# Performance work log

Hardware: AMD Instinct MI355X
Metric: run time of the kernel (lower is better)

The kernel has to match this reference:

```python
import jax, jax.numpy as jnp
import numpy as np

N_NODES = 100000


def gcn_layer(x, W, b, src, dst, n):
    # PyG GCNConv: add self-loops, symmetric degree normalization,
    # message = norm * (x @ W)[src], aggregated (sum) at dst, plus bias.
    loops = jnp.arange(n, dtype=src.dtype)
    s = jnp.concatenate([src, loops])  # [E+N]
    d = jnp.concatenate([dst, loops])  # [E+N]
    deg = jnp.zeros((n,), x.dtype).at[d].add(jnp.ones((s.shape[0],), x.dtype))
    dinv = jnp.where(deg > 0, jax.lax.rsqrt(deg), 0.0)
    norm = dinv[s] * dinv[d]  # [E+N]
    h = x @ W  # [N, out]
    msg = h[s] * norm[:, None]  # [E+N, out]
    out = jax.ops.segment_sum(msg, d, num_segments=n)
    return out + b


def setup_inputs() -> dict:
    key = jax.random.key(0)
    k1, k2, k3, k4 = jax.random.split(key, 4)
    in_dim, hid_dim, out_dim = 128, 128, 64
    x = jax.random.normal(k1, (N_NODES, in_dim), dtype=jnp.float32)
    edge_index = jax.random.randint(k2, (2, 1600000), 0, N_NODES, dtype=jnp.int64)
    W1 = jax.random.normal(k3, (in_dim, hid_dim), dtype=jnp.float32) / np.sqrt(in_dim)
    b1 = jnp.zeros((hid_dim,), jnp.float32)
    W2 = jax.random.normal(k4, (hid_dim, out_dim), dtype=jnp.float32) / np.sqrt(hid_dim)
    b2 = jnp.zeros((out_dim,), jnp.float32)
    return {"x": x, "edge_index": edge_index, "W1": W1, "b1": b1, "W2": W2, "b2": b2}


def reference(x, edge_index, W1, b1, W2, b2):
    src, dst = edge_index[0], edge_index[1]
    h = gcn_layer(x, W1, b1, src, dst, N_NODES)
    h = jax.nn.relu(h)
    # F.dropout(training=False) -> identity (eval mode reference)
    out = gcn_layer(h, W2, b2, src, dst, N_NODES)
    return out
```

## Files before the change

kernel.cpp:

```cpp
#include <hip/hip_runtime.h>
#include <hip/hip_fp16.h>

#define NN 100000
#define NSB 256
#define WPS2 391
#define CAP2 8192
#define EPB 16

typedef _Float16 f16;
typedef _Float16 f16x8 __attribute__((ext_vector_type(8)));
typedef float f32x4 __attribute__((ext_vector_type(4)));

__device__ __forceinline__ int eload(const void* e, long i, int is64) {
  if (is64) return (int)((const long long*)e)[i];
  return ((const int*)e)[i];
}

__global__ __launch_bounds__(1024) void k_detect(const unsigned* __restrict__ e,
                                                 int* __restrict__ flag,
                                                 int* __restrict__ bcur2) {
  __shared__ unsigned red[1024];
  int t = threadIdx.x;
  if (t < NSB) bcur2[t] = t * CAP2;
  unsigned acc = e[1 + 2 * t] | e[1 + 2 * t + 2048];
  red[t] = acc;
  __syncthreads();
  for (int off = 512; off > 0; off >>= 1) {
    if (t < off) red[t] |= red[t + off];
    __syncthreads();
  }
  if (t == 0) *flag = (red[0] == 0) ? 1 : 0;
}

__global__ void k_wprep(const float* __restrict__ W1, const float* __restrict__ W2,
                        f16* __restrict__ Wt1, f16* __restrict__ Wt2) {
  int idx = blockIdx.x * 256 + threadIdx.x;
  if (idx < 128 * 128) {
    int k = idx / 128, n = idx % 128;
    Wt1[n * 128 + k] = (f16)W1[idx];
  } else {
    int i2 = idx - 128 * 128;
    if (i2 < 128 * 64) {
      int k = i2 / 64, n = i2 % 64;
      Wt2[n * 128 + k] = (f16)W2[i2];
    }
  }
}

__global__ __launch_bounds__(256) void k_split(const void* __restrict__ e,
                                               const int* __restrict__ flag,
                                               int E, int* __restrict__ bcur2,
                                               int* __restrict__ srcb,
                                               int* __restrict__ dstb) {
  __shared__ int hist[NSB];
  const int tid = threadIdx.x;
  const long b0 = (long)blockIdx.x * (256 * EPB);
  const int is64 = *flag;
  hist[tid] = 0;
  __syncthreads();

  int sv[EPB], dv[EPB];
#pragma unroll
  for (int j = 0; j < EPB; ++j) {
    long idx = b0 + j * 256 + tid;
    int s = 0, d = -1;
    if (idx < E) {
      s = eload(e, idx, is64);
      d = eload(e, (long)E + idx, is64);
    }
    sv[j] = s; dv[j] = d;
    if (d >= 0) atomicAdd(&hist[(unsigned)d / WPS2], 1);
  }
  __syncthreads();
  {
    int c = hist[tid];
    int base = (c > 0) ? atomicAdd(&bcur2[tid], c) : 0;
    __syncthreads();
    hist[tid] = base;
  }
  __syncthreads();
#pragma unroll
  for (int j = 0; j < EPB; ++j) {
    int d = dv[j];
    if (d < 0) continue;
    int pos = atomicAdd(&hist[(unsigned)d / WPS2], 1);
    srcb[pos] = sv[j];
    dstb[pos] = d;
  }
}

__global__ __launch_bounds__(256) void k_wscan(const int* __restrict__ bcur2,
                                               int* __restrict__ wbase,
                                               int* __restrict__ rowptr, int E) {
  __shared__ int sm[NSB];
  int t = threadIdx.x;
  int c = bcur2[t] - t * CAP2;
  sm[t] = c;
  __syncthreads();
  for (int off = 1; off < NSB; off <<= 1) {
    int a = (t >= off) ? sm[t - off] : 0;
    __syncthreads();
    sm[t] += a;
    __syncthreads();
  }
  wbase[t] = sm[t] - c;
  if (t == 0) rowptr[NN] = E;
}

__global__ __launch_bounds__(256) void k_build(const int* __restrict__ dstb,
                                               const int* __restrict__ srcb,
                                               const int* __restrict__ bcur2,
                                               const int* __restrict__ wbase,
                                               int* __restrict__ rowptr,
                                               float* __restrict__ dinv,
                                               int* __restrict__ csr) {
  __shared__ int lc[512];
  __shared__ int cur[512];
  const int tid = threadIdx.x;
  const int b = blockIdx.x;
  const int nlo = b * WPS2;
  const int nhi = (nlo + WPS2 < NN) ? nlo + WPS2 : NN;
  const int nw = nhi - nlo;
  lc[tid] = 0; lc[tid + 256] = 0;
  __syncthreads();
  const int cnt = bcur2[b] - b * CAP2;
  const long s0 = (long)b * CAP2;
  for (int i = tid; i < cnt; i += 256)
    atomicAdd(&lc[dstb[s0 + i] - nlo], 1);
  __syncthreads();
  for (int off = 1; off < 512; off <<= 1) {
    int a0 = (tid >= off) ? lc[tid - off] : 0;
    int a1 = (tid + 256 >= off) ? lc[tid + 256 - off] : 0;
    __syncthreads();
    lc[tid] += a0; lc[tid + 256] += a1;
    __syncthreads();
  }
  const int wb = wbase[b];
#pragma unroll
  for (int h = 0; h < 2; ++h) {
    int j = tid + h * 256;
    if (j < nw) {
      int inc = lc[j];
      int c = inc - (j > 0 ? lc[j - 1] : 0);
      int ex = wb + inc - c;
      rowptr[nlo + j] = ex;
      dinv[nlo + j] = rsqrtf((float)c + 1.0f);
      cur[j] = ex;
    }
  }
  __syncthreads();
  for (int i = tid; i < cnt; i += 256) {
    int d = dstb[s0 + i];
    int pos = atomicAdd(&cur[d - nlo], 1);
    csr[pos] = srcb[s0 + i];
  }
}

template <int COUT, bool RELU, typename TIN>
__global__ __launch_bounds__(256) void gemm_mfma(const TIN* __restrict__ X,
                                                 const f16* __restrict__ Wt,
                                                 const float* __restrict__ dinv,
                                                 f16* __restrict__ Y) {
  constexpr int NF = COUT / 16;
  __shared__ f16 Al[128 * 128];
  __shared__ f16 Bl[COUT * 128];
  const int tid = threadIdx.x;
  const long row0 = (long)blockIdx.x * 128;

  for (int c = tid; c < COUT * 16; c += 256) {
    int n = c >> 4, g = c & 15;
    f16x8 v = *(const f16x8*)&Wt[n * 128 + g * 8];
    *(f16x8*)((char*)Bl + n * 256 + ((g * 16) ^ ((n & 7) << 4))) = v;
  }
  for (int c = tid; c < 2048; c += 256) {
    int r = c >> 4, g = c & 15;
    long grow = row0 + r;
    f16x8 v;
    if (grow < NN) {
      if constexpr (sizeof(TIN) == 4) {
        const float4* p = (const float4*)&X[grow * 128 + g * 8];
        float4 p0 = p[0], p1 = p[1];
        float f[8] = {p0.x, p0.y, p0.z, p0.w, p1.x, p1.y, p1.z, p1.w};
#pragma unroll
        for (int j = 0; j < 8; ++j) {
          float t = RELU ? fmaxf(f[j], 0.f) : f[j];
          v[j] = (f16)t;
        }
      } else {
        v = *(const f16x8*)&X[grow * 128 + g * 8];
        if (RELU) {
#pragma unroll
          for (int j = 0; j < 8; ++j) v[j] = v[j] > (f16)0 ? v[j] : (f16)0;
        }
      }
    } else {
#pragma unroll
      for (int j = 0; j < 8; ++j) v[j] = (f16)0;
    }
    *(f16x8*)((char*)Al + r * 256 + ((g * 16) ^ ((r & 7) << 4))) = v;
  }
  __syncthreads();

  const int l = tid & 63, w = tid >> 6;
  const int lm = l & 15, lg = l >> 4;
  const int r0 = w * 32 + lm, r1 = r0 + 16;

  f32x4 acc0[NF], acc1[NF];
#pragma unroll
  for (int nf = 0; nf < NF; ++nf) { acc0[nf] = (f32x4)(0.f); acc1[nf] = (f32x4)(0.f); }

#pragma unroll
  for (int kk = 0; kk < 4; ++kk) {
    const int kb = kk * 64 + lg * 16;
    f16x8 a0 = *(const f16x8*)((const char*)Al + r0 * 256 + (kb ^ ((r0 & 7) << 4)));
    f16x8 a1 = *(const f16x8*)((const char*)Al + r1 * 256 + (kb ^ ((r1 & 7) << 4)));
#pragma unroll
    for (int nf = 0; nf < NF; ++nf) {
      int n = nf * 16 + lm;
      f16x8 b = *(const f16x8*)((const char*)Bl + n * 256 + (kb ^ ((n & 7) << 4)));
      acc0[nf] = __builtin_amdgcn_mfma_f32_16x16x32_f16(a0, b, acc0[nf], 0, 0, 0);
      acc1[nf] = __builtin_amdgcn_mfma_f32_16x16x32_f16(a1, b, acc1[nf], 0, 0, 0);
    }
  }

#pragma unroll
  for (int reg = 0; reg < 4; ++reg) {
    long gr0 = row0 + w * 32 + lg * 4 + reg;
    long gr1 = gr0 + 16;
    float d0 = (gr0 < NN) ? dinv[gr0] : 0.f;
    float d1 = (gr1 < NN) ? dinv[gr1] : 0.f;
#pragma unroll
    for (int nf = 0; nf < NF; ++nf) {
      if (gr0 < NN) Y[gr0 * COUT + nf * 16 + lm] = (f16)(acc0[nf][reg] * d0);
      if (gr1 < NN) Y[gr1 * COUT + nf * 16 + lm] = (f16)(acc1[nf][reg] * d1);
    }
  }
}

__device__ __forceinline__ void acc8f(float* acc, const __half* p) {
  float4 raw = *(const float4*)p;
  const __half2* h = (const __half2*)&raw;
#pragma unroll
  for (int q = 0; q < 4; ++q) {
    float2 f = __half22float2(h[q]);
    acc[2 * q] += f.x; acc[2 * q + 1] += f.y;
  }
}

template <int C, typename TOUT>
__global__ __launch_bounds__(256) void k_agg8(const __half* __restrict__ hn,
                                              const int* __restrict__ rowptr,
                                              const int* __restrict__ csr,
                                              const float* __restrict__ dinv,
                                              const float* __restrict__ bias,
                                              TOUT* __restrict__ out) {
  constexpr int TP = C / 8;
  long t = (long)blockIdx.x * 256 + threadIdx.x;
  int d = (int)(t / TP);
  if (d >= NN) return;
  int c8 = (int)(t % TP) * 8;

  float acc[8] = {0, 0, 0, 0, 0, 0, 0, 0};
  acc8f(acc, &hn[(long)d * C + c8]);
  int e = rowptr[d];
  const int end = rowptr[d + 1];

  for (; e + 8 <= end; e += 8) {
    int s[8];
#pragma unroll
    for (int u = 0; u < 8; ++u) s[u] = csr[e + u];
    float4 r[8];
#pragma unroll
    for (int u = 0; u < 8; ++u) r[u] = *(const float4*)&hn[(long)s[u] * C + c8];
#pragma unroll
    for (int u = 0; u < 8; ++u) {
      const __half2* h = (const __half2*)&r[u];
#pragma unroll
      for (int q = 0; q < 4; ++q) {
        float2 f = __half22float2(h[q]);
        acc[2 * q] += f.x; acc[2 * q + 1] += f.y;
      }
    }
  }
  if (e + 4 <= end) {
    int s[4];
#pragma unroll
    for (int u = 0; u < 4; ++u) s[u] = csr[e + u];
    float4 r[4];
#pragma unroll
    for (int u = 0; u < 4; ++u) r[u] = *(const float4*)&hn[(long)s[u] * C + c8];
#pragma unroll
    for (int u = 0; u < 4; ++u) {
      const __half2* h = (const __half2*)&r[u];
#pragma unroll
      for (int q = 0; q < 4; ++q) {
        float2 f = __half22float2(h[q]);
        acc[2 * q] += f.x; acc[2 * q + 1] += f.y;
      }
    }
    e += 4;
  }
  for (; e < end; ++e) acc8f(acc, &hn[(long)csr[e] * C + c8]);

  float dd = dinv[d];
  float4 bv0 = *(const float4*)&bias[c8];
  float4 bv1 = *(const float4*)&bias[c8 + 4];
  float o[8];
  o[0] = acc[0] * dd + bv0.x; o[1] = acc[1] * dd + bv0.y;
  o[2] = acc[2] * dd + bv0.z; o[3] = acc[3] * dd + bv0.w;
  o[4] = acc[4] * dd + bv1.x; o[5] = acc[5] * dd + bv1.y;
  o[6] = acc[6] * dd + bv1.z; o[7] = acc[7] * dd + bv1.w;

  if constexpr (sizeof(TOUT) == 2) {
    __half2 hp[4];
    hp[0] = __floats2half2_rn(o[0], o[1]);
    hp[1] = __floats2half2_rn(o[2], o[3]);
    hp[2] = __floats2half2_rn(o[4], o[5]);
    hp[3] = __floats2half2_rn(o[6], o[7]);
    *(float4*)&out[(long)d * C + c8] = *(float4*)hp;
  } else {
    *(float4*)&out[(long)d * C + c8]     = make_float4(o[0], o[1], o[2], o[3]);
    *(float4*)&out[(long)d * C + c8 + 4] = make_float4(o[4], o[5], o[6], o[7]);
  }
}

extern "C" void kernel_launch(void* const* d_in, const int* in_sizes, int n_in,
                              void* d_out, int out_size, void* d_ws, size_t ws_size,
                              hipStream_t stream) {
  const float* x  = (const float*)d_in[0];
  const void*  ep = d_in[1];
  const float* W1 = (const float*)d_in[2];
  const float* b1 = (const float*)d_in[3];
  const float* W2 = (const float*)d_in[4];
  const float* b2 = (const float*)d_in[5];
  float* out = (float*)d_out;
  const int E = in_sizes[1] / 2;

  float*  wsf    = (float*)d_ws;
  int*    wsi    = (int*)d_ws;
  int*    flag   = wsi;
  int*    bcur2  = wsi + 64;
  int*    wbase  = wsi + 320;
  float*  dinv   = wsf + 576;
  int*    rowptr = wsi + 100576;
  f16*    Wt1    = (f16*)(wsi + 200640);
  f16*    Wt2    = (f16*)(wsi + 208832);
  int*    csr    = wsi + 212992;
  int*    srcb   = wsi + 1812992;
  int*    dstb   = wsi + 3910144;
  f16*    hn1    = (f16*)(wsi + 6007296);
  f16*    a1     = (f16*)(wsi + 12407296);
  f16*    hn2    = hn1;

  const int SB = (E + 256 * EPB - 1) / (256 * EPB);
  const int GB = (NN + 127) / 128;

  k_detect<<<1, 1024, 0, stream>>>((const unsigned*)ep, flag, bcur2);
  k_wprep<<<96, 256, 0, stream>>>(W1, W2, Wt1, Wt2);
  k_split<<<SB, 256, 0, stream>>>(ep, flag, E, bcur2, srcb, dstb);
  k_wscan<<<1, 256, 0, stream>>>(bcur2, wbase, rowptr, E);
  k_build<<<NSB, 256, 0, stream>>>(dstb, srcb, bcur2, wbase, rowptr, dinv, csr);

  gemm_mfma<128, false, float><<<GB, 256, 0, stream>>>(x, Wt1, dinv, hn1);
  k_agg8<128, __half><<<(NN * 16 + 255) / 256, 256, 0, stream>>>(
      (const __half*)hn1, rowptr, csr, dinv, b1, (__half*)a1);

  gemm_mfma<64, true, f16><<<GB, 256, 0, stream>>>(a1, Wt2, dinv, hn2);
  k_agg8<64, float><<<(NN * 8 + 255) / 256, 256, 0, stream>>>(
      (const __half*)hn2, rowptr, csr, dinv, b2, out);
}
```

Baseline: 196.1 us.

## Split aggregation into column slices so each thread covers eight channels

The aggregation kernels now split the feature dimension into 8 column slices, one per block: each slice is 16 channels in layer 1 and 8 channels in layer 2. Every thread still handles 8 channels, but a block now processes many more destination rows for one narrow slice. Consecutive blocks cover different slices of the same rows. Gathered hn rows are fetched as 16- or 32-byte pieces instead of full rows, which may improve cache locality per slice but fragments each gathered row into more, smaller accesses.

```diff
diff --git a/kernel.cpp b/kernel.cpp
--- a/kernel.cpp
+++ b/kernel.cpp
@@ -237,31 +237,27 @@
   }
 }
 
-__device__ __forceinline__ void acc8f(float* acc, const __half* p) {
-  float4 raw = *(const float4*)p;
-  const __half2* h = (const __half2*)&raw;
-#pragma unroll
-  for (int q = 0; q < 4; ++q) {
-    float2 f = __half22float2(h[q]);
-    acc[2 * q] += f.x; acc[2 * q + 1] += f.y;
-  }
-}
-
-template <int C, typename TOUT>
-__global__ __launch_bounds__(256) void k_agg8(const __half* __restrict__ hn,
+template <int C, int SCH, typename TOUT>
+__global__ __launch_bounds__(256) void k_aggs(const f16* __restrict__ hn,
                                               const int* __restrict__ rowptr,
                                               const int* __restrict__ csr,
                                               const float* __restrict__ dinv,
                                               const float* __restrict__ bias,
                                               TOUT* __restrict__ out) {
-  constexpr int TP = C / 8;
-  long t = (long)blockIdx.x * 256 + threadIdx.x;
-  int d = (int)(t / TP);
+  constexpr int TP = SCH / 8;
+  constexpr int RPB = 256 / TP;
+  const int slice = blockIdx.x & 7;
+  const int tid = threadIdx.x;
+  const long d = (long)(blockIdx.x >> 3) * RPB + tid / TP;
   if (d >= NN) return;
-  int c8 = (int)(t % TP) * 8;
-
-  float acc[8] = {0, 0, 0, 0, 0, 0, 0, 0};
-  acc8f(acc, &hn[(long)d * C + c8]);
+  const int c8 = slice * SCH + (tid % TP) * 8;
+
+  float acc[8];
+  {
+    f16x8 v = *(const f16x8*)&hn[d * C + c8];
+#pragma unroll
+    for (int j = 0; j < 8; ++j) acc[j] = (float)v[j];
+  }
   int e = rowptr[d];
   const int end = rowptr[d + 1];
 
@@ -269,58 +265,49 @@
     int s[8];
 #pragma unroll
     for (int u = 0; u < 8; ++u) s[u] = csr[e + u];
-    float4 r[8];
-#pragma unroll
-    for (int u = 0; u < 8; ++u) r[u] = *(const float4*)&hn[(long)s[u] * C + c8];
-#pragma unroll
-    for (int u = 0; u < 8; ++u) {
-      const __half2* h = (const __half2*)&r[u];
-#pragma unroll
-      for (int q = 0; q < 4; ++q) {
-        float2 f = __half22float2(h[q]);
-        acc[2 * q] += f.x; acc[2 * q + 1] += f.y;
-      }
-    }
+    f16x8 r[8];
+#pragma unroll
+    for (int u = 0; u < 8; ++u) r[u] = *(const f16x8*)&hn[(long)s[u] * C + c8];
+#pragma unroll
+    for (int u = 0; u < 8; ++u)
+#pragma unroll
+      for (int j = 0; j < 8; ++j) acc[j] += (float)r[u][j];
   }
   if (e + 4 <= end) {
     int s[4];
 #pragma unroll
     for (int u = 0; u < 4; ++u) s[u] = csr[e + u];
-    float4 r[4];
-#pragma unroll
-    for (int u = 0; u < 4; ++u) r[u] = *(const float4*)&hn[(long)s[u] * C + c8];
-#pragma unroll
-    for (int u = 0; u < 4; ++u) {
-      const __half2* h = (const __half2*)&r[u];
-#pragma unroll
-      for (int q = 0; q < 4; ++q) {
-        float2 f = __half22float2(h[q]);
-        acc[2 * q] += f.x; acc[2 * q + 1] += f.y;
-      }
-    }
+    f16x8 r[4];
+#pragma unroll
+    for (int u = 0; u < 4; ++u) r[u] = *(const f16x8*)&hn[(long)s[u] * C + c8];
+#pragma unroll
+    for (int u = 0; u < 4; ++u)
+#pragma unroll
+      for (int j = 0; j < 8; ++j) acc[j] += (float)r[u][j];
     e += 4;
   }
-  for (; e < end; ++e) acc8f(acc, &hn[(long)csr[e] * C + c8]);
+  for (; e < end; ++e) {
+    f16x8 r0 = *(const f16x8*)&hn[(long)csr[e] * C + c8];
+#pragma unroll
+    for (int j = 0; j < 8; ++j) acc[j] += (float)r0[j];
+  }
 
   float dd = dinv[d];
   float4 bv0 = *(const float4*)&bias[c8];
   float4 bv1 = *(const float4*)&bias[c8 + 4];
+  const float bb[8] = {bv0.x, bv0.y, bv0.z, bv0.w, bv1.x, bv1.y, bv1.z, bv1.w};
   float o[8];
-  o[0] = acc[0] * dd + bv0.x; o[1] = acc[1] * dd + bv0.y;
-  o[2] = acc[2] * dd + bv0.z; o[3] = acc[3] * dd + bv0.w;
-  o[4] = acc[4] * dd + bv1.x; o[5] = acc[5] * dd + bv1.y;
-  o[6] = acc[6] * dd + bv1.z; o[7] = acc[7] * dd + bv1.w;
+#pragma unroll
+  for (int j = 0; j < 8; ++j) o[j] = acc[j] * dd + bb[j];
 
   if constexpr (sizeof(TOUT) == 2) {
-    __half2 hp[4];
-    hp[0] = __floats2half2_rn(o[0], o[1]);
-    hp[1] = __floats2half2_rn(o[2], o[3]);
-    hp[2] = __floats2half2_rn(o[4], o[5]);
-    hp[3] = __floats2half2_rn(o[6], o[7]);
-    *(float4*)&out[(long)d * C + c8] = *(float4*)hp;
+    f16x8 hv;
+#pragma unroll
+    for (int j = 0; j < 8; ++j) hv[j] = (f16)o[j];
+    *(f16x8*)&out[d * C + c8] = hv;
   } else {
-    *(float4*)&out[(long)d * C + c8]     = make_float4(o[0], o[1], o[2], o[3]);
-    *(float4*)&out[(long)d * C + c8 + 4] = make_float4(o[4], o[5], o[6], o[7]);
+    *(float4*)&out[d * C + c8]     = make_float4(o[0], o[1], o[2], o[3]);
+    *(float4*)&out[d * C + c8 + 4] = make_float4(o[4], o[5], o[6], o[7]);
   }
 }
 
@@ -362,10 +349,14 @@
   k_build<<<NSB, 256, 0, stream>>>(dstb, srcb, bcur2, wbase, rowptr, dinv, csr);
 
   gemm_mfma<128, false, float><<<GB, 256, 0, stream>>>(x, Wt1, dinv, hn1);
-  k_agg8<128, __half><<<(NN * 16 + 255) / 256, 256, 0, stream>>>(
-      (const __half*)hn1, rowptr, csr, dinv, b1, (__half*)a1);
+  {
+    const int AB = 8 * ((NN + 127) / 128);
+    k_aggs<128, 16, f16><<<AB, 256, 0, stream>>>(hn1, rowptr, csr, dinv, b1, a1);
+  }
 
   gemm_mfma<64, true, f16><<<GB, 256, 0, stream>>>(a1, Wt2, dinv, hn2);
-  k_agg8<64, float><<<(NN * 8 + 255) / 256, 256, 0, stream>>>(
-      (const __half*)hn2, rowptr, csr, dinv, b2, out);
-}
+  {
+    const int AB = 8 * ((NN + 255) / 256);
+    k_aggs<64, 8, float><<<AB, 256, 0, stream>>>(hn2, rowptr, csr, dinv, b2, out);
+  }
+}
```

After: 520.3 us. 165% more time.

## Pack edge buckets into one word, pad bucket counters, merge prep kernels

Applied to the files above, without the earlier changes.

Packs each bucketed edge's local destination offset and source index into a single 32-bit word, halving the intermediate bucket traffic between the split and build kernels. Pads the per-bucket atomic counters to separate cache lines to reduce contention, and merges the detect and weight-prep kernels into one launch. Also uses nontemporal loads for CSR indices and nontemporal stores for the final output. The packing relies on source indices fitting in 17 bits and local offsets in the remaining bits, which holds for 100000 nodes.

```diff
diff --git a/kernel.cpp b/kernel.cpp
--- a/kernel.cpp
+++ b/kernel.cpp
@@ -16,33 +16,36 @@
   return ((const int*)e)[i];
 }
 
-__global__ __launch_bounds__(1024) void k_detect(const unsigned* __restrict__ e,
-                                                 int* __restrict__ flag,
-                                                 int* __restrict__ bcur2) {
-  __shared__ unsigned red[1024];
-  int t = threadIdx.x;
-  if (t < NSB) bcur2[t] = t * CAP2;
-  unsigned acc = e[1 + 2 * t] | e[1 + 2 * t + 2048];
-  red[t] = acc;
-  __syncthreads();
-  for (int off = 512; off > 0; off >>= 1) {
-    if (t < off) red[t] |= red[t + off];
-    __syncthreads();
-  }
-  if (t == 0) *flag = (red[0] == 0) ? 1 : 0;
-}
-
-__global__ void k_wprep(const float* __restrict__ W1, const float* __restrict__ W2,
-                        f16* __restrict__ Wt1, f16* __restrict__ Wt2) {
-  int idx = blockIdx.x * 256 + threadIdx.x;
-  if (idx < 128 * 128) {
-    int k = idx / 128, n = idx % 128;
-    Wt1[n * 128 + k] = (f16)W1[idx];
+__global__ __launch_bounds__(1024) void k_prep(const unsigned* __restrict__ e,
+                                               int* __restrict__ flag,
+                                               int* __restrict__ bcur2,
+                                               const float* __restrict__ W1,
+                                               const float* __restrict__ W2,
+                                               f16* __restrict__ Wt1,
+                                               f16* __restrict__ Wt2) {
+  const int t = threadIdx.x;
+  if (blockIdx.x == 0) {
+    __shared__ unsigned red[1024];
+    if (t < NSB) bcur2[t * 16] = t * CAP2;
+    unsigned acc = e[1 + 2 * t] | e[1 + 2 * t + 2048];
+    red[t] = acc;
+    __syncthreads();
+    for (int off = 512; off > 0; off >>= 1) {
+      if (t < off) red[t] |= red[t + off];
+      __syncthreads();
+    }
+    if (t == 0) *flag = (red[0] == 0) ? 1 : 0;
   } else {
-    int i2 = idx - 128 * 128;
-    if (i2 < 128 * 64) {
-      int k = i2 / 64, n = i2 % 64;
-      Wt2[n * 128 + k] = (f16)W2[i2];
+    int idx = (blockIdx.x - 1) * 1024 + t;
+    if (idx < 128 * 128) {
+      int k = idx / 128, n = idx % 128;
+      Wt1[n * 128 + k] = (f16)W1[idx];
+    } else {
+      int i2 = idx - 128 * 128;
+      if (i2 < 128 * 64) {
+        int k = i2 / 64, n = i2 % 64;
+        Wt2[n * 128 + k] = (f16)W2[i2];
+      }
     }
   }
 }
@@ -50,8 +53,7 @@
 __global__ __launch_bounds__(256) void k_split(const void* __restrict__ e,
                                                const int* __restrict__ flag,
                                                int E, int* __restrict__ bcur2,
-                                               int* __restrict__ srcb,
-                                               int* __restrict__ dstb) {
+                                               int* __restrict__ pk) {
   __shared__ int hist[NSB];
   const int tid = threadIdx.x;
   const long b0 = (long)blockIdx.x * (256 * EPB);
@@ -74,7 +76,7 @@
   __syncthreads();
   {
     int c = hist[tid];
-    int base = (c > 0) ? atomicAdd(&bcur2[tid], c) : 0;
+    int base = (c > 0) ? atomicAdd(&bcur2[tid * 16], c) : 0;
     __syncthreads();
     hist[tid] = base;
   }
@@ -83,9 +85,10 @@
   for (int j = 0; j < EPB; ++j) {
     int d = dv[j];
     if (d < 0) continue;
-    int pos = atomicAdd(&hist[(unsigned)d / WPS2], 1);
-    srcb[pos] = sv[j];
-    dstb[pos] = d;
+    int w = (unsigned)d / WPS2;
+    int dloc = d - w * WPS2;
+    int pos = atomicAdd(&hist[w], 1);
+    pk[pos] = (dloc << 17) | sv[j];
   }
 }
 
@@ -94,7 +97,7 @@
                                                int* __restrict__ rowptr, int E) {
   __shared__ int sm[NSB];
   int t = threadIdx.x;
-  int c = bcur2[t] - t * CAP2;
+  int c = bcur2[t * 16] - t * CAP2;
   sm[t] = c;
   __syncthreads();
   for (int off = 1; off < NSB; off <<= 1) {
@@ -107,8 +110,7 @@
   if (t == 0) rowptr[NN] = E;
 }
 
-__global__ __launch_bounds__(256) void k_build(const int* __restrict__ dstb,
-                                               const int* __restrict__ srcb,
+__global__ __launch_bounds__(256) void k_build(const int* __restrict__ pk,
                                                const int* __restrict__ bcur2,
                                                const int* __restrict__ wbase,
                                                int* __restrict__ rowptr,
@@ -123,10 +125,10 @@
   const int nw = nhi - nlo;
   lc[tid] = 0; lc[tid + 256] = 0;
   __syncthreads();
-  const int cnt = bcur2[b] - b * CAP2;
+  const int cnt = bcur2[b * 16] - b * CAP2;
   const long s0 = (long)b * CAP2;
   for (int i = tid; i < cnt; i += 256)
-    atomicAdd(&lc[dstb[s0 + i] - nlo], 1);
+    atomicAdd(&lc[(unsigned)pk[s0 + i] >> 17], 1);
   __syncthreads();
   for (int off = 1; off < 512; off <<= 1) {
     int a0 = (tid >= off) ? lc[tid - off] : 0;
@@ -150,9 +152,9 @@
   }
   __syncthreads();
   for (int i = tid; i < cnt; i += 256) {
-    int d = dstb[s0 + i];
-    int pos = atomicAdd(&cur[d - nlo], 1);
-    csr[pos] = srcb[s0 + i];
+    int p = pk[s0 + i];
+    int pos = atomicAdd(&cur[(unsigned)p >> 17], 1);
+    csr[pos] = p & 0x1FFFF;
   }
 }
 
@@ -268,7 +270,7 @@
   for (; e + 8 <= end; e += 8) {
     int s[8];
 #pragma unroll
-    for (int u = 0; u < 8; ++u) s[u] = csr[e + u];
+    for (int u = 0; u < 8; ++u) s[u] = __builtin_nontemporal_load(csr + e + u);
     float4 r[8];
 #pragma unroll
     for (int u = 0; u < 8; ++u) r[u] = *(const float4*)&hn[(long)s[u] * C + c8];
@@ -285,7 +287,7 @@
   if (e + 4 <= end) {
     int s[4];
 #pragma unroll
-    for (int u = 0; u < 4; ++u) s[u] = csr[e + u];
+    for (int u = 0; u < 4; ++u) s[u] = __builtin_nontemporal_load(csr + e + u);
     float4 r[4];
 #pragma unroll
     for (int u = 0; u < 4; ++u) r[u] = *(const float4*)&hn[(long)s[u] * C + c8];
@@ -300,7 +302,7 @@
     }
     e += 4;
   }
-  for (; e < end; ++e) acc8f(acc, &hn[(long)csr[e] * C + c8]);
+  for (; e < end; ++e) acc8f(acc, &hn[(long)__builtin_nontemporal_load(csr + e) * C + c8]);
 
   float dd = dinv[d];
   float4 bv0 = *(const float4*)&bias[c8];
@@ -319,8 +321,10 @@
     hp[3] = __floats2half2_rn(o[6], o[7]);
     *(float4*)&out[(long)d * C + c8] = *(float4*)hp;
   } else {
-    *(float4*)&out[(long)d * C + c8]     = make_float4(o[0], o[1], o[2], o[3]);
-    *(float4*)&out[(long)d * C + c8 + 4] = make_float4(o[4], o[5], o[6], o[7]);
+    f32x4 v0 = {o[0], o[1], o[2], o[3]};
+    f32x4 v1 = {o[4], o[5], o[6], o[7]};
+    __builtin_nontemporal_store(v0, (f32x4*)&out[(long)d * C + c8]);
+    __builtin_nontemporal_store(v1, (f32x4*)&out[(long)d * C + c8 + 4]);
   }
 }
 
@@ -340,26 +344,24 @@
   int*    wsi    = (int*)d_ws;
   int*    flag   = wsi;
   int*    bcur2  = wsi + 64;
-  int*    wbase  = wsi + 320;
-  float*  dinv   = wsf + 576;
-  int*    rowptr = wsi + 100576;
-  f16*    Wt1    = (f16*)(wsi + 200640);
-  f16*    Wt2    = (f16*)(wsi + 208832);
-  int*    csr    = wsi + 212992;
-  int*    srcb   = wsi + 1812992;
-  int*    dstb   = wsi + 3910144;
-  f16*    hn1    = (f16*)(wsi + 6007296);
-  f16*    a1     = (f16*)(wsi + 12407296);
+  int*    wbase  = wsi + 4224;
+  float*  dinv   = wsf + 4480;
+  int*    rowptr = wsi + 104480;
+  f16*    Wt1    = (f16*)(wsi + 204496);
+  f16*    Wt2    = (f16*)(wsi + 212688);
+  int*    csr    = wsi + 216784;
+  int*    pk     = wsi + 1816784;
+  f16*    hn1    = (f16*)(wsi + 3913936);
+  f16*    a1     = (f16*)(wsi + 10313936);
   f16*    hn2    = hn1;
 
   const int SB = (E + 256 * EPB - 1) / (256 * EPB);
   const int GB = (NN + 127) / 128;
 
-  k_detect<<<1, 1024, 0, stream>>>((const unsigned*)ep, flag, bcur2);
-  k_wprep<<<96, 256, 0, stream>>>(W1, W2, Wt1, Wt2);
-  k_split<<<SB, 256, 0, stream>>>(ep, flag, E, bcur2, srcb, dstb);
+  k_prep<<<25, 1024, 0, stream>>>((const unsigned*)ep, flag, bcur2, W1, W2, Wt1, Wt2);
+  k_split<<<SB, 256, 0, stream>>>(ep, flag, E, bcur2, pk);
   k_wscan<<<1, 256, 0, stream>>>(bcur2, wbase, rowptr, E);
-  k_build<<<NSB, 256, 0, stream>>>(dstb, srcb, bcur2, wbase, rowptr, dinv, csr);
+  k_build<<<NSB, 256, 0, stream>>>(pk, bcur2, wbase, rowptr, dinv, csr);
 
   gemm_mfma<128, false, float><<<GB, 256, 0, stream>>>(x, Wt1, dinv, hn1);
   k_agg8<128, __half><<<(NN * 16 + 255) / 256, 256, 0, stream>>>(
```

Measured after the change: 226.6 us. 1.16x slower.
